# Kernel optimization log

Measured on AMD Instinct MI355X. Metric: run time of the kernel, lower is better.

The kernel has to match this reference:

```python
import jax, jax.numpy as jnp
import numpy as np

B, T, D, H = 4, 2048, 1024, 16
HD = D // H  # 64


def setup_inputs() -> dict:
    key = jax.random.key(0)
    ks = jax.random.split(key, 9)
    s = 1.0 / np.sqrt(D)
    return {
        "x": jax.random.normal(ks[0], (B, T, D), dtype=jnp.float32),
        "Wq": jax.random.normal(ks[1], (D, D), dtype=jnp.float32) * s,
        "bq": jnp.zeros((D,), dtype=jnp.float32),
        "Wk": jax.random.normal(ks[2], (D, D), dtype=jnp.float32) * s,
        "bk": jnp.zeros((D,), dtype=jnp.float32),
        "Wv": jax.random.normal(ks[3], (D, D), dtype=jnp.float32) * s,
        "bv": jnp.zeros((D,), dtype=jnp.float32),
        "Wo": jax.random.normal(ks[4], (D, D), dtype=jnp.float32) * s,
        "bo": jnp.zeros((D,), dtype=jnp.float32),
    }


def reference(x, Wq, bq, Wk, bk, Wv, bv, Wo, bo):
    Bx, Tx, C = x.shape
    # QKV projections -> (B, H, T, HD)
    q = (x @ Wq + bq).reshape(Bx, Tx, H, HD).transpose(0, 2, 1, 3)
    k = (x @ Wk + bk).reshape(Bx, Tx, H, HD).transpose(0, 2, 1, 3)
    v = (x @ Wv + bv).reshape(Bx, Tx, H, HD).transpose(0, 2, 1, 3)
    # scaled dot-product scores (B, H, T, T)
    scores = jnp.einsum("bhqd,bhkd->bhqk", q, k) / jnp.sqrt(jnp.float32(HD))
    causal = jnp.tril(jnp.ones((Tx, Tx), dtype=bool))
    scores = jnp.where(causal[None, None, :, :], scores, jnp.float32(-1e9))
    attn = jax.nn.softmax(scores, axis=-1)
    out = jnp.einsum("bhqk,bhkd->bhqd", attn, v)  # (B, H, T, HD)
    out = out.transpose(0, 2, 1, 3).reshape(Bx, Tx, C)
    return out @ Wo + bo
```

## Files before the change

### kernel.cpp

```cpp
#include <hip/hip_runtime.h>


#define B_  4
#define T_  2048
#define D_  1024
#define H_  16
#define HD_ 64
#define M_  (B_ * T_)

typedef __bf16 bf16x8 __attribute__((ext_vector_type(8)));
typedef float  floatx4 __attribute__((ext_vector_type(4)));

__device__ __forceinline__ unsigned short f2b(float f) {
  unsigned int u = __float_as_uint(f);
  unsigned int r = (u + 0x7fffu + ((u >> 16) & 1u)) >> 16;
  return (unsigned short)r;
}

__device__ __forceinline__ float fast_exp2(float x) {
#if __has_builtin(__builtin_amdgcn_exp2f)
  return __builtin_amdgcn_exp2f(x);
#else
  return exp2f(x);
#endif
}

__device__ __forceinline__ void async_ld16(const void* g, void* l) {
  __builtin_amdgcn_global_load_lds(
      (const __attribute__((address_space(1))) void*)g,
      (__attribute__((address_space(3))) void*)l, 16, 0, 0);
}


__global__ void cast_fp32_to_bf16(const float* __restrict__ in,
                                  unsigned short* __restrict__ out, int n) {
  int i = (blockIdx.x * 256 + threadIdx.x) * 4;
  if (i >= n) return;
  float4 v = *(const float4*)(in + i);
  ushort4 o;
  o.x = f2b(v.x); o.y = f2b(v.y); o.z = f2b(v.z); o.w = f2b(v.w);
  *(ushort4*)(out + i) = o;
}

__global__ void transpose_cast(const float* __restrict__ W0, const float* __restrict__ W1,
                               const float* __restrict__ W2, const float* __restrict__ W3,
                               unsigned short* __restrict__ O0, unsigned short* __restrict__ O1,
                               unsigned short* __restrict__ O2, unsigned short* __restrict__ O3) {
  __shared__ float tile[32][33];
  int z = blockIdx.z;
  const float* W = z == 0 ? W0 : z == 1 ? W1 : z == 2 ? W2 : W3;
  unsigned short* O = z == 0 ? O0 : z == 1 ? O1 : z == 2 ? O2 : O3;
  int n0 = blockIdx.x * 32, k0 = blockIdx.y * 32;
  int tx = threadIdx.x, ty = threadIdx.y;
#pragma unroll
  for (int i = 0; i < 4; ++i)
    tile[ty + i * 8][tx] = W[(size_t)(k0 + ty + i * 8) * D_ + n0 + tx];
  __syncthreads();
#pragma unroll
  for (int i = 0; i < 4; ++i)
    O[(size_t)(n0 + ty + i * 8) * D_ + k0 + tx] = f2b(tile[tx][ty + i * 8]);
}


__global__ __launch_bounds__(256, 2)
void gemm_qkv(const unsigned short* __restrict__ A,
              const unsigned short* __restrict__ Wt,
              const float* __restrict__ bq, const float* __restrict__ bk,
              const float* __restrict__ bv,
              unsigned short* __restrict__ Qo, unsigned short* __restrict__ Ko,
              unsigned short* __restrict__ Vo) {
  __shared__ __align__(16) unsigned short As[128 * 64];
  __shared__ __align__(16) unsigned short Bs[128 * 64];
  const int K = D_;

  const int tid = threadIdx.x;
  const int wave = tid >> 6, lane = tid & 63;
  const int quad = lane >> 4, l16 = lane & 15;
  const int m0 = blockIdx.y * 128, n0 = blockIdx.x * 128;
  const int wm = (wave >> 1) * 64, wn = (wave & 1) * 64;

  const int rsub = lane >> 3;
  const int csw = ((lane & 7) ^ rsub) * 8;
  const int rw = wave * 32;

  const unsigned short* Ag = A + (size_t)(m0 + rw + rsub) * K + csw;
  const unsigned short* Bg = Wt + (size_t)(n0 + rw + rsub) * K + csw;

  floatx4 acc[4][4] = {};

  for (int kt = 0; kt < K; kt += 64) {
#pragma unroll
    for (int j = 0; j < 4; ++j) {
      async_ld16(Ag + (size_t)(j * 8) * K + kt, &As[(rw + j * 8) * 64]);
      async_ld16(Bg + (size_t)(j * 8) * K + kt, &Bs[(rw + j * 8) * 64]);
    }
    __syncthreads();

#pragma unroll
    for (int kk = 0; kk < 2; ++kk) {
      bf16x8 a[4], b[4];
#pragma unroll
      for (int i = 0; i < 4; ++i) {
        const int ra = wm + i * 16 + l16;
        a[i] = *(const bf16x8*)&As[ra * 64 + (((kk * 4 + quad) ^ (ra & 7)) * 8)];
      }
#pragma unroll
      for (int i = 0; i < 4; ++i) {
        const int rb = wn + i * 16 + l16;
        b[i] = *(const bf16x8*)&Bs[rb * 64 + (((kk * 4 + quad) ^ (rb & 7)) * 8)];
      }
#pragma unroll
      for (int mi = 0; mi < 4; ++mi)
#pragma unroll
        for (int ni = 0; ni < 4; ++ni)
          acc[mi][ni] = __builtin_amdgcn_mfma_f32_16x16x32_bf16(
              a[mi], b[ni], acc[mi][ni], 0, 0, 0);
    }
    __syncthreads();
  }

  const int which = n0 >> 10;
  const float* bias = which == 0 ? bq : which == 1 ? bk : bv;
  unsigned short* Out = which == 0 ? Qo : which == 1 ? Ko : Vo;

#pragma unroll
  for (int mi = 0; mi < 4; ++mi) {
#pragma unroll
    for (int ni = 0; ni < 4; ++ni) {
#pragma unroll
      for (int r = 0; r < 4; ++r) {
        const int m = m0 + wm + mi * 16 + quad * 4 + r;
        const int n = n0 + wn + ni * 16 + l16;
        const float val = acc[mi][ni][r] + bias[n & 1023];
        const int b = m >> 11, t = m & (T_ - 1);
        const int nl = n & 1023;
        const int h = nl >> 6, d = nl & (HD_ - 1);
        size_t idx;
        if (which == 2) {
          const int tp = (t & ~63) | (((t & 15) << 2) | ((t >> 4) & 3));
          idx = ((size_t)(b * H_ + h) * HD_ + d) * T_ + tp;
        } else {
          idx = ((size_t)(b * H_ + h) * T_ + t) * HD_ + d;
        }
        Out[idx] = f2b(val);
      }
    }
  }
}


__global__ __launch_bounds__(256, 2)
void gemm_out(const unsigned short* __restrict__ A,
              const unsigned short* __restrict__ Bt,
              const float* __restrict__ bias,
              float* __restrict__ Cout, int N, int K) {
  __shared__ __align__(16) unsigned short As[128 * 64];
  __shared__ __align__(16) unsigned short Bs[128 * 64];

  const int tid = threadIdx.x;
  const int wave = tid >> 6, lane = tid & 63;
  const int quad = lane >> 4, l16 = lane & 15;
  const int m0 = blockIdx.y * 128, n0 = blockIdx.x * 128;
  const int wm = (wave >> 1) * 64, wn = (wave & 1) * 64;

  const int rsub = lane >> 3;
  const int csw = ((lane & 7) ^ rsub) * 8;
  const int rw = wave * 32;

  const unsigned short* Ag = A + (size_t)(m0 + rw + rsub) * K + csw;
  const unsigned short* Bg = Bt + (size_t)(n0 + rw + rsub) * K + csw;

  floatx4 acc[4][4] = {};

  for (int kt = 0; kt < K; kt += 64) {
#pragma unroll
    for (int j = 0; j < 4; ++j) {
      async_ld16(Ag + (size_t)(j * 8) * K + kt, &As[(rw + j * 8) * 64]);
      async_ld16(Bg + (size_t)(j * 8) * K + kt, &Bs[(rw + j * 8) * 64]);
    }
    __syncthreads();

#pragma unroll
    for (int kk = 0; kk < 2; ++kk) {
      bf16x8 a[4], b[4];
#pragma unroll
      for (int i = 0; i < 4; ++i) {
        const int ra = wm + i * 16 + l16;
        a[i] = *(const bf16x8*)&As[ra * 64 + (((kk * 4 + quad) ^ (ra & 7)) * 8)];
      }
#pragma unroll
      for (int i = 0; i < 4; ++i) {
        const int rb = wn + i * 16 + l16;
        b[i] = *(const bf16x8*)&Bs[rb * 64 + (((kk * 4 + quad) ^ (rb & 7)) * 8)];
      }
#pragma unroll
      for (int mi = 0; mi < 4; ++mi)
#pragma unroll
        for (int ni = 0; ni < 4; ++ni)
          acc[mi][ni] = __builtin_amdgcn_mfma_f32_16x16x32_bf16(
              a[mi], b[ni], acc[mi][ni], 0, 0, 0);
    }
    __syncthreads();
  }

#pragma unroll
  for (int mi = 0; mi < 4; ++mi)
#pragma unroll
    for (int ni = 0; ni < 4; ++ni)
#pragma unroll
      for (int r = 0; r < 4; ++r) {
        const int m = m0 + wm + mi * 16 + quad * 4 + r;
        const int n = n0 + wn + ni * 16 + l16;
        Cout[(size_t)m * N + n] = acc[mi][ni][r] + bias[n];
      }
}


#define PSTR 72

template <bool MASKED>
__device__ __forceinline__ void attn_chunk64(
    int kbse, int qw, int quad, int l16,
    const unsigned short* __restrict__ Ks,
    const unsigned short* __restrict__ Vs,
    const bf16x8 (&aq)[4][2], floatx4 (&o)[4][4], floatx4 (&lacc)[4],
    unsigned short* __restrict__ plw,
    bf16x8 vones) {
  const int sw = l16 & 7;

  bf16x8 kf0[4], kf1[4];
#pragma unroll
  for (int j = 0; j < 4; ++j) {
    const unsigned short* kr = &Ks[(j * 16 + l16) * HD_];
    kf0[j] = *(const bf16x8*)&kr[(quad ^ sw) * 8];
    kf1[j] = *(const bf16x8*)&kr[((quad + 4) ^ sw) * 8];
  }

  const float SL = 0.125f * 1.44269504f;
  const float CB = 8.0f * 1.44269504f;

#pragma unroll
  for (int qt = 0; qt < 4; ++qt) {
    floatx4 s[4] = {};
#pragma unroll
    for (int j = 0; j < 4; ++j) {
      s[j] = __builtin_amdgcn_mfma_f32_16x16x32_bf16(aq[qt][0], kf0[j], s[j], 0, 0, 0);
      s[j] = __builtin_amdgcn_mfma_f32_16x16x32_bf16(aq[qt][1], kf1[j], s[j], 0, 0, 0);
    }
    unsigned short* pw = plw + qt * (16 * PSTR);
#pragma unroll
    for (int r = 0; r < 4; ++r) {
      float v0 = s[0][r], v1 = s[1][r], v2 = s[2][r], v3 = s[3][r];
      if (MASKED) {
        const int qrow = qw + qt * 16 + quad * 4 + r;
        if (kbse + l16 > qrow)      v0 = -1e30f;
        if (kbse + 16 + l16 > qrow) v1 = -1e30f;
        if (kbse + 32 + l16 > qrow) v2 = -1e30f;
        if (kbse + 48 + l16 > qrow) v3 = -1e30f;
      }
      const float p0 = fast_exp2(__builtin_fmaf(v0, SL, -CB));
      const float p1 = fast_exp2(__builtin_fmaf(v1, SL, -CB));
      const float p2 = fast_exp2(__builtin_fmaf(v2, SL, -CB));
      const float p3 = fast_exp2(__builtin_fmaf(v3, SL, -CB));
      uint2 pk;
      pk.x = __builtin_amdgcn_perm(__float_as_uint(p1), __float_as_uint(p0), 0x07060302u);
      pk.y = __builtin_amdgcn_perm(__float_as_uint(p3), __float_as_uint(p2), 0x07060302u);
      *(uint2*)&pw[(quad * 4 + r) * PSTR + 4 * l16] = pk;
    }
  }

  bf16x8 vf0[4], vf1[4];
#pragma unroll
  for (int d4 = 0; d4 < 4; ++d4) {
    const unsigned short* vr = &Vs[(d4 * 16 + l16) * 64];
    vf0[d4] = *(const bf16x8*)&vr[(quad ^ sw) * 8];
    vf1[d4] = *(const bf16x8*)&vr[((quad + 4) ^ sw) * 8];
  }

#pragma unroll
  for (int qt = 0; qt < 4; ++qt) {
    const unsigned short* pw = plw + qt * (16 * PSTR);
    const bf16x8 pf0 = *(const bf16x8*)&pw[l16 * PSTR + quad * 8];
    const bf16x8 pf1 = *(const bf16x8*)&pw[l16 * PSTR + 32 + quad * 8];
    lacc[qt] = __builtin_amdgcn_mfma_f32_16x16x32_bf16(pf0, vones, lacc[qt], 0, 0, 0);
    lacc[qt] = __builtin_amdgcn_mfma_f32_16x16x32_bf16(pf1, vones, lacc[qt], 0, 0, 0);
#pragma unroll
    for (int d4 = 0; d4 < 4; ++d4) {
      o[qt][d4] = __builtin_amdgcn_mfma_f32_16x16x32_bf16(pf0, vf0[d4], o[qt][d4], 0, 0, 0);
      o[qt][d4] = __builtin_amdgcn_mfma_f32_16x16x32_bf16(pf1, vf1[d4], o[qt][d4], 0, 0, 0);
    }
  }
}

__global__ __launch_bounds__(256, 2)
void attn_kernel(const unsigned short* __restrict__ Q,
                 const unsigned short* __restrict__ K,
                 const unsigned short* __restrict__ Vp,
                 unsigned short* __restrict__ O) {
  __shared__ __align__(16) unsigned short Ks[64 * HD_];
  __shared__ __align__(16) unsigned short Vs[HD_ * 64];
  __shared__ unsigned short Pl[4][4][16 * PSTR];

  const int bidx = blockIdx.x;
  const int xcd = bidx & 7;
  const int i = bidx >> 3;
  const int bh_local = i & 7;
  const int g = i >> 3;
  const int kg = (g < 4) ? g : 11 - g;
  const int bh = (xcd << 3) | bh_local;

  const int wave = threadIdx.x >> 6, lane = threadIdx.x & 63;
  const int quad = lane >> 4, l16 = lane & 15;
  const int tile = kg * 4 + wave;
  const int qw = tile * 64;

  const unsigned short* Qb = Q + (size_t)bh * T_ * HD_;
  const unsigned short* Kb = K + (size_t)bh * T_ * HD_;
  const unsigned short* Vb = Vp + (size_t)bh * HD_ * T_;

  bf16x8 aq[4][2];
#pragma unroll
  for (int qt = 0; qt < 4; ++qt) {
    const unsigned short* qp = Qb + (size_t)(qw + qt * 16 + l16) * HD_;
    aq[qt][0] = *(const bf16x8*)(qp + quad * 8);
    aq[qt][1] = *(const bf16x8*)(qp + 32 + quad * 8);
  }

  union { unsigned short u[8]; bf16x8 v8; } ones;
#pragma unroll
  for (int i2 = 0; i2 < 8; ++i2) ones.u[i2] = 0x3F80;

  floatx4 o[4][4] = {};
  floatx4 lacc[4] = {};

  const int rsub = lane >> 3;
  const int csw = ((lane & 7) ^ rsub) * 8;
  const int rA = 8 * wave;
  const int rB = 8 * (wave + 4);

  const int my_nfull = tile;
  const int nit = 4 * kg + 4;

  for (int kc = 0; kc < nit; ++kc) {
    const int kbse = kc * 64;
    if (kc) __syncthreads();
    async_ld16(Kb + (size_t)(kbse + rA + rsub) * HD_ + csw, &Ks[rA * HD_]);
    async_ld16(Kb + (size_t)(kbse + rB + rsub) * HD_ + csw, &Ks[rB * HD_]);
    async_ld16(Vb + (size_t)(rA + rsub) * T_ + kbse + csw, &Vs[rA * 64]);
    async_ld16(Vb + (size_t)(rB + rsub) * T_ + kbse + csw, &Vs[rB * 64]);
    __syncthreads();

    if (kc < my_nfull)
      attn_chunk64<false>(kbse, qw, quad, l16, Ks, Vs, aq, o, lacc,
                          &Pl[wave][0][0], ones.v8);
    else if (kc == my_nfull)
      attn_chunk64<true>(kbse, qw, quad, l16, Ks, Vs, aq, o, lacc,
                         &Pl[wave][0][0], ones.v8);
  }

  const int b = bh >> 4, h = bh & 15;
#pragma unroll
  for (int qt = 0; qt < 4; ++qt) {
#pragma unroll
    for (int r = 0; r < 4; ++r) {
      const float inv = 1.0f / lacc[qt][r];
      const int tt = qw + qt * 16 + quad * 4 + r;
      unsigned short* orow = O + (size_t)(b * T_ + tt) * D_ + h * HD_;
      orow[l16]      = f2b(o[qt][0][r] * inv);
      orow[16 + l16] = f2b(o[qt][1][r] * inv);
      orow[32 + l16] = f2b(o[qt][2][r] * inv);
      orow[48 + l16] = f2b(o[qt][3][r] * inv);
    }
  }
}


extern "C" void kernel_launch(void* const* d_in, const int* in_sizes, int n_in,
                              void* d_out, int out_size, void* d_ws, size_t ws_size,
                              hipStream_t stream) {
  const float* x  = (const float*)d_in[0];
  const float* Wq = (const float*)d_in[1];
  const float* bq = (const float*)d_in[2];
  const float* Wk = (const float*)d_in[3];
  const float* bk = (const float*)d_in[4];
  const float* Wv = (const float*)d_in[5];
  const float* bv = (const float*)d_in[6];
  const float* Wo = (const float*)d_in[7];
  const float* bo = (const float*)d_in[8];
  float* out = (float*)d_out;

  char* ws = (char*)d_ws;
  const size_t MB = 1u << 20;
  unsigned short* xb  = (unsigned short*)(ws);
  unsigned short* Wqt = (unsigned short*)(ws + 16 * MB);
  unsigned short* Wkt = (unsigned short*)(ws + 18 * MB);
  unsigned short* Wvt = (unsigned short*)(ws + 20 * MB);
  unsigned short* Wot = (unsigned short*)(ws + 22 * MB);
  unsigned short* Qb  = (unsigned short*)(ws + 24 * MB);
  unsigned short* Kb  = (unsigned short*)(ws + 40 * MB);
  unsigned short* Vtb = (unsigned short*)(ws + 56 * MB);
  unsigned short* Ob  = xb;

  cast_fp32_to_bf16<<<dim3(M_ * D_ / 1024), dim3(256), 0, stream>>>(x, xb, M_ * D_);
  transpose_cast<<<dim3(32, 32, 4), dim3(32, 8), 0, stream>>>(
      Wq, Wk, Wv, Wo, Wqt, Wkt, Wvt, Wot);

  gemm_qkv<<<dim3(24, M_ / 128), dim3(256), 0, stream>>>(
      xb, Wqt, bq, bk, bv, Qb, Kb, Vtb);

  attn_kernel<<<dim3(512), dim3(256), 0, stream>>>(Qb, Kb, Vtb, Ob);

  gemm_out<<<dim3(D_ / 128, M_ / 128), dim3(256), 0, stream>>>(
      Ob, Wot, bo, out, D_, D_);
}
```

Baseline: 264.8 us.

## Double-buffer K/V tiles in attention loop and prefetch next chunk

The K and V shared-memory tiles become two buffers. The loads for chunk kc+1 are issued right after the loop-top barrier, so they overlap with compute on chunk kc, and each iteration needs one barrier instead of two. To keep LDS within budget at the same occupancy, the per-wave P staging buffer is cut from four 16-row slots to two, and the chunk is processed in two halves. This adds ordering constraints on P-slot reuse within a wave, and correctness relies on the barrier waiting for the outstanding async LDS loads.

```diff
diff --git a/kernel.cpp b/kernel.cpp
--- a/kernel.cpp
+++ b/kernel.cpp
@@ -224,9 +224,11 @@
     const unsigned short* __restrict__ Ks,
     const unsigned short* __restrict__ Vs,
     const bf16x8 (&aq)[4][2], floatx4 (&o)[4][4], floatx4 (&lacc)[4],
-    unsigned short* __restrict__ plw,
+    unsigned short* __restrict__ pl0, unsigned short* __restrict__ pl1,
     bf16x8 vones) {
   const int sw = l16 & 7;
+  const float SL = 0.125f * 1.44269504f;
+  const float CB = 8.0f * 1.44269504f;
 
   bf16x8 kf0[4], kf1[4];
 #pragma unroll
@@ -236,58 +238,63 @@
     kf1[j] = *(const bf16x8*)&kr[((quad + 4) ^ sw) * 8];
   }
 
-  const float SL = 0.125f * 1.44269504f;
-  const float CB = 8.0f * 1.44269504f;
-
-#pragma unroll
-  for (int qt = 0; qt < 4; ++qt) {
-    floatx4 s[4] = {};
-#pragma unroll
-    for (int j = 0; j < 4; ++j) {
-      s[j] = __builtin_amdgcn_mfma_f32_16x16x32_bf16(aq[qt][0], kf0[j], s[j], 0, 0, 0);
-      s[j] = __builtin_amdgcn_mfma_f32_16x16x32_bf16(aq[qt][1], kf1[j], s[j], 0, 0, 0);
-    }
-    unsigned short* pw = plw + qt * (16 * PSTR);
-#pragma unroll
-    for (int r = 0; r < 4; ++r) {
-      float v0 = s[0][r], v1 = s[1][r], v2 = s[2][r], v3 = s[3][r];
-      if (MASKED) {
-        const int qrow = qw + qt * 16 + quad * 4 + r;
-        if (kbse + l16 > qrow)      v0 = -1e30f;
-        if (kbse + 16 + l16 > qrow) v1 = -1e30f;
-        if (kbse + 32 + l16 > qrow) v2 = -1e30f;
-        if (kbse + 48 + l16 > qrow) v3 = -1e30f;
-      }
-      const float p0 = fast_exp2(__builtin_fmaf(v0, SL, -CB));
-      const float p1 = fast_exp2(__builtin_fmaf(v1, SL, -CB));
-      const float p2 = fast_exp2(__builtin_fmaf(v2, SL, -CB));
-      const float p3 = fast_exp2(__builtin_fmaf(v3, SL, -CB));
-      uint2 pk;
-      pk.x = __builtin_amdgcn_perm(__float_as_uint(p1), __float_as_uint(p0), 0x07060302u);
-      pk.y = __builtin_amdgcn_perm(__float_as_uint(p3), __float_as_uint(p2), 0x07060302u);
-      *(uint2*)&pw[(quad * 4 + r) * PSTR + 4 * l16] = pk;
-    }
-  }
-
   bf16x8 vf0[4], vf1[4];
-#pragma unroll
-  for (int d4 = 0; d4 < 4; ++d4) {
-    const unsigned short* vr = &Vs[(d4 * 16 + l16) * 64];
-    vf0[d4] = *(const bf16x8*)&vr[(quad ^ sw) * 8];
-    vf1[d4] = *(const bf16x8*)&vr[((quad + 4) ^ sw) * 8];
-  }
-
-#pragma unroll
-  for (int qt = 0; qt < 4; ++qt) {
-    const unsigned short* pw = plw + qt * (16 * PSTR);
-    const bf16x8 pf0 = *(const bf16x8*)&pw[l16 * PSTR + quad * 8];
-    const bf16x8 pf1 = *(const bf16x8*)&pw[l16 * PSTR + 32 + quad * 8];
-    lacc[qt] = __builtin_amdgcn_mfma_f32_16x16x32_bf16(pf0, vones, lacc[qt], 0, 0, 0);
-    lacc[qt] = __builtin_amdgcn_mfma_f32_16x16x32_bf16(pf1, vones, lacc[qt], 0, 0, 0);
-#pragma unroll
-    for (int d4 = 0; d4 < 4; ++d4) {
-      o[qt][d4] = __builtin_amdgcn_mfma_f32_16x16x32_bf16(pf0, vf0[d4], o[qt][d4], 0, 0, 0);
-      o[qt][d4] = __builtin_amdgcn_mfma_f32_16x16x32_bf16(pf1, vf1[d4], o[qt][d4], 0, 0, 0);
+
+#pragma unroll
+  for (int half = 0; half < 2; ++half) {
+#pragma unroll
+    for (int i = 0; i < 2; ++i) {
+      const int qt = half * 2 + i;
+      unsigned short* pw = i ? pl1 : pl0;
+      floatx4 s[4] = {};
+#pragma unroll
+      for (int j = 0; j < 4; ++j) {
+        s[j] = __builtin_amdgcn_mfma_f32_16x16x32_bf16(aq[qt][0], kf0[j], s[j], 0, 0, 0);
+        s[j] = __builtin_amdgcn_mfma_f32_16x16x32_bf16(aq[qt][1], kf1[j], s[j], 0, 0, 0);
+      }
+#pragma unroll
+      for (int r = 0; r < 4; ++r) {
+        float v0 = s[0][r], v1 = s[1][r], v2 = s[2][r], v3 = s[3][r];
+        if (MASKED) {
+          const int qrow = qw + qt * 16 + quad * 4 + r;
+          if (kbse + l16 > qrow)      v0 = -1e30f;
+          if (kbse + 16 + l16 > qrow) v1 = -1e30f;
+          if (kbse + 32 + l16 > qrow) v2 = -1e30f;
+          if (kbse + 48 + l16 > qrow) v3 = -1e30f;
+        }
+        const float p0 = fast_exp2(__builtin_fmaf(v0, SL, -CB));
+        const float p1 = fast_exp2(__builtin_fmaf(v1, SL, -CB));
+        const float p2 = fast_exp2(__builtin_fmaf(v2, SL, -CB));
+        const float p3 = fast_exp2(__builtin_fmaf(v3, SL, -CB));
+        uint2 pk;
+        pk.x = __builtin_amdgcn_perm(__float_as_uint(p1), __float_as_uint(p0), 0x07060302u);
+        pk.y = __builtin_amdgcn_perm(__float_as_uint(p3), __float_as_uint(p2), 0x07060302u);
+        *(uint2*)&pw[(quad * 4 + r) * PSTR + 4 * l16] = pk;
+      }
+    }
+
+    if (half == 0) {
+#pragma unroll
+      for (int d4 = 0; d4 < 4; ++d4) {
+        const unsigned short* vr = &Vs[(d4 * 16 + l16) * 64];
+        vf0[d4] = *(const bf16x8*)&vr[(quad ^ sw) * 8];
+        vf1[d4] = *(const bf16x8*)&vr[((quad + 4) ^ sw) * 8];
+      }
+    }
+
+#pragma unroll
+    for (int i = 0; i < 2; ++i) {
+      const int qt = half * 2 + i;
+      const unsigned short* pw = i ? pl1 : pl0;
+      const bf16x8 pf0 = *(const bf16x8*)&pw[l16 * PSTR + quad * 8];
+      const bf16x8 pf1 = *(const bf16x8*)&pw[l16 * PSTR + 32 + quad * 8];
+      lacc[qt] = __builtin_amdgcn_mfma_f32_16x16x32_bf16(pf0, vones, lacc[qt], 0, 0, 0);
+      lacc[qt] = __builtin_amdgcn_mfma_f32_16x16x32_bf16(pf1, vones, lacc[qt], 0, 0, 0);
+#pragma unroll
+      for (int d4 = 0; d4 < 4; ++d4) {
+        o[qt][d4] = __builtin_amdgcn_mfma_f32_16x16x32_bf16(pf0, vf0[d4], o[qt][d4], 0, 0, 0);
+        o[qt][d4] = __builtin_amdgcn_mfma_f32_16x16x32_bf16(pf1, vf1[d4], o[qt][d4], 0, 0, 0);
+      }
     }
   }
 }
@@ -297,9 +304,9 @@
                  const unsigned short* __restrict__ K,
                  const unsigned short* __restrict__ Vp,
                  unsigned short* __restrict__ O) {
-  __shared__ __align__(16) unsigned short Ks[64 * HD_];
-  __shared__ __align__(16) unsigned short Vs[HD_ * 64];
-  __shared__ unsigned short Pl[4][4][16 * PSTR];
+  __shared__ __align__(16) unsigned short Ks[2][64 * HD_];
+  __shared__ __align__(16) unsigned short Vs[2][HD_ * 64];
+  __shared__ unsigned short Pl[4][2][16 * PSTR];
 
   const int bidx = blockIdx.x;
   const int xcd = bidx & 7;
@@ -341,21 +348,34 @@
   const int my_nfull = tile;
   const int nit = 4 * kg + 4;
 
+  async_ld16(Kb + (size_t)(rA + rsub) * HD_ + csw, &Ks[0][rA * HD_]);
+  async_ld16(Kb + (size_t)(rB + rsub) * HD_ + csw, &Ks[0][rB * HD_]);
+  async_ld16(Vb + (size_t)(rA + rsub) * T_ + csw, &Vs[0][rA * 64]);
+  async_ld16(Vb + (size_t)(rB + rsub) * T_ + csw, &Vs[0][rB * 64]);
+
   for (int kc = 0; kc < nit; ++kc) {
+    __syncthreads();
+
+    const int nk = kc + 1;
+    if (nk < nit) {
+      const int kn = nk * 64;
+      unsigned short* Kn = Ks[nk & 1];
+      unsigned short* Vn = Vs[nk & 1];
+      async_ld16(Kb + (size_t)(kn + rA + rsub) * HD_ + csw, &Kn[rA * HD_]);
+      async_ld16(Kb + (size_t)(kn + rB + rsub) * HD_ + csw, &Kn[rB * HD_]);
+      async_ld16(Vb + (size_t)(rA + rsub) * T_ + kn + csw, &Vn[rA * 64]);
+      async_ld16(Vb + (size_t)(rB + rsub) * T_ + kn + csw, &Vn[rB * 64]);
+    }
+
+    const unsigned short* Kc = Ks[kc & 1];
+    const unsigned short* Vc = Vs[kc & 1];
     const int kbse = kc * 64;
-    if (kc) __syncthreads();
-    async_ld16(Kb + (size_t)(kbse + rA + rsub) * HD_ + csw, &Ks[rA * HD_]);
-    async_ld16(Kb + (size_t)(kbse + rB + rsub) * HD_ + csw, &Ks[rB * HD_]);
-    async_ld16(Vb + (size_t)(rA + rsub) * T_ + kbse + csw, &Vs[rA * 64]);
-    async_ld16(Vb + (size_t)(rB + rsub) * T_ + kbse + csw, &Vs[rB * 64]);
-    __syncthreads();
-
     if (kc < my_nfull)
-      attn_chunk64<false>(kbse, qw, quad, l16, Ks, Vs, aq, o, lacc,
-                          &Pl[wave][0][0], ones.v8);
+      attn_chunk64<false>(kbse, qw, quad, l16, Kc, Vc, aq, o, lacc,
+                          &Pl[wave][0][0], &Pl[wave][1][0], ones.v8);
     else if (kc == my_nfull)
-      attn_chunk64<true>(kbse, qw, quad, l16, Ks, Vs, aq, o, lacc,
-                         &Pl[wave][0][0], ones.v8);
+      attn_chunk64<true>(kbse, qw, quad, l16, Kc, Vc, aq, o, lacc,
+                         &Pl[wave][0][0], &Pl[wave][1][0], ones.v8);
   }
 
   const int b = bh >> 4, h = bh & 15;
```

New measurement: 263.3 us. Within noise of the previous version (-0.6%).
